# Kernel tuning notes

Hardware: AMD Instinct MI355X
Metric: run time of the kernel (lower is better)

Reference implementation:

```python
import jax, jax.numpy as jnp
import numpy as np

B = 4096
N_WIRES = 4
N_OPS = 8
# fixed (control, target) wire pairs for the 8 'random' two-qubit CRY gates
PAIRS = [(0, 1), (1, 2), (2, 3), (3, 0), (0, 2), (1, 3), (2, 0), (3, 1)]
AX = "abcd"  # einsum letters for the 4 qubit axes


def _cry(theta):
    """Controlled-RY gate as a [2,2,2,2] tensor (c_out, t_out, c_in, t_in). Real-valued."""
    c, s = jnp.cos(theta / 2), jnp.sin(theta / 2)
    ry = jnp.stack([jnp.stack([c, -s]), jnp.stack([s, c])])  # [2,2]
    G = jnp.zeros((2, 2, 2, 2), dtype=ry.dtype)
    G = G.at[0, :, 0, :].set(jnp.eye(2, dtype=ry.dtype))
    G = G.at[1, :, 1, :].set(ry)
    return G


def _apply_2q(state, G, c, t):
    """Apply 2-qubit gate G to qubits (c, t) of state [N,2,2,2,2]."""
    out = list(AX)
    out[c], out[t] = "x", "y"
    spec = f"xy{AX[c]}{AX[t]},n{AX}->n{''.join(out)}"
    return jnp.einsum(spec, G, state)


def _quanv(x, theta):
    """Batched 4-qubit state-vector sim over all 196 2x2 patches at once."""
    bsz = x.shape[0]
    img = x.reshape(bsz, 28, 28)
    # [B,14,14,2,2] patches; flatten row-major gives [x[r,c], x[r,c+1], x[r+1,c], x[r+1,c+1]]
    patches = img.reshape(bsz, 14, 2, 14, 2).transpose(0, 1, 3, 2, 4)
    angles = patches.reshape(bsz * 196, 4)  # [N,4] RY angles
    # RY(theta)|0> = cos(t/2)|0> + sin(t/2)|1>  -> product state over 4 wires
    amp = jnp.stack([jnp.cos(angles / 2), jnp.sin(angles / 2)], axis=-1)  # [N,4,2]
    state = jnp.einsum("na,nb,nc,nd->nabcd", amp[:, 0], amp[:, 1], amp[:, 2], amp[:, 3])
    # 8 fixed-pattern parameterized CRY gates (RandomLayer analogue; all-real so state stays real)
    for k, (cw, tw) in enumerate(PAIRS):
        state = _apply_2q(state, _cry(theta[k]), cw, tw)
    probs = state ** 2  # real amplitudes -> |amp|^2
    z = jnp.array([1.0, -1.0], dtype=state.dtype)
    meas = jnp.stack([jnp.einsum(f"n{AX},{AX[w]}->n", probs, z) for w in range(N_WIRES)], axis=-1)
    return meas.reshape(bsz, 196 * 4)  # [B,784], patch-major layout matches torch cat


def setup_inputs() -> dict:
    key = jax.random.key(0)
    ks = jax.random.split(key, 11)
    x = jax.random.uniform(ks[0], (B, 1, 28, 28), dtype=jnp.float32)
    theta = jax.random.uniform(ks[1], (N_OPS,), dtype=jnp.float32, minval=0.0, maxval=2.0 * np.pi)
    s = 0.05
    W1 = jax.random.normal(ks[2], (784, 512), jnp.float32) * s
    b1 = jnp.zeros((512,), jnp.float32)
    W2 = jax.random.normal(ks[3], (512, 32), jnp.float32) * s
    b2 = jnp.zeros((32,), jnp.float32)
    W3 = jax.random.normal(ks[4], (32, 512), jnp.float32) * s
    b3 = jnp.zeros((512,), jnp.float32)
    W4 = jax.random.normal(ks[5], (512, 784), jnp.float32) * s
    b4 = jnp.zeros((784,), jnp.float32)
    return dict(x=x, theta=theta, W1=W1, b1=b1, W2=W2, b2=b2, W3=W3, b3=b3, W4=W4, b4=b4)


def reference(x, theta, W1, b1, W2, b2, W3, b3, W4, b4):
    feats = _quanv(x, theta)                          # [B,784]
    h = jax.nn.relu(feats @ W1 + b1)                  # encoder
    latent = h @ W2 + b2                              # [B,32]
    h2 = jax.nn.relu(latent @ W3 + b3)                # decoder
    recon = jax.nn.sigmoid(h2 @ W4 + b4)              # [B,784]
    return recon.reshape(x.shape[0], 1, 28, 28)
```

## Files before the change

kernel.cpp:

```cpp
#include <hip/hip_runtime.h>
#include <hip/hip_bf16.h>
#include <math.h>


#define BATCH   4096
#define NPATCH  196
#define FEATDIM 784
#define KP1     896
#define NP4     832

typedef __bf16 b8 __attribute__((ext_vector_type(8)));
typedef float  f4 __attribute__((ext_vector_type(4)));

__device__ __forceinline__ unsigned short f2bf(float f) {
    unsigned u = __float_as_uint(f);
    u += 0x7FFF + ((u >> 16) & 1);
    return (unsigned short)(u >> 16);
}

__device__ __forceinline__ void gload16(const void* g, void* l) {
    __builtin_amdgcn_global_load_lds(
        (const __attribute__((address_space(1))) unsigned int*)g,
        (__attribute__((address_space(3))) unsigned int*)l, 16, 0, 0);
}

#define Q_END   3136
#define T1_END  3248
#define T4_END  3352
#define W2T_END 3416
#define W3T_END 3480
#define ZF_END  3704

__global__ __launch_bounds__(256)
void prep_kernel(const float* __restrict__ x, const float* __restrict__ theta,
                 const float* __restrict__ W1, const float* __restrict__ W2,
                 const float* __restrict__ W3, const float* __restrict__ W4,
                 unsigned short* __restrict__ featsB,
                 unsigned short* __restrict__ W1B,
                 unsigned short* __restrict__ W4B,
                 unsigned short* __restrict__ W2T,
                 unsigned short* __restrict__ W3T) {
    __shared__ float shm[64 * 65];
    const int bid = blockIdx.x;
    const int tid = threadIdx.x;

    if (bid < Q_END) {
        float (*Us)[16] = (float (*)[16])shm;
        if (tid < 16) {
            const int cb[8] = {3, 2, 1, 0, 3, 2, 1, 0};
            const int tb[8] = {2, 1, 0, 3, 1, 0, 3, 2};
            float v[16];
#pragma unroll
            for (int s = 0; s < 16; ++s) v[s] = (s == tid) ? 1.0f : 0.0f;
            for (int k = 0; k < 8; ++k) {
                float th = theta[k] * 0.5f;
                float ct, st;
                __sincosf(th, &st, &ct);
                int cm = 1 << cb[k], tm = 1 << tb[k];
#pragma unroll
                for (int s = 0; s < 16; ++s) {
                    if ((s & cm) && !(s & tm)) {
                        float v0 = v[s], v1 = v[s | tm];
                        v[s]      = ct * v0 - st * v1;
                        v[s | tm] = st * v0 + ct * v1;
                    }
                }
            }
#pragma unroll
            for (int s = 0; s < 16; ++s) Us[s][tid] = v[s];
        }
        __syncthreads();

        int n = bid * 256 + tid;
        int b = n / NPATCH;
        int p = n % NPATCH;
        int r = p / 14;
        int c = p % 14;

        const float* img = x + (size_t)b * FEATDIM;
        float2 p0 = *(const float2*)&img[(2 * r) * 28 + 2 * c];
        float2 p1 = *(const float2*)&img[(2 * r + 1) * 28 + 2 * c];

        float amp[4][2];
        __sincosf(p0.x * 0.5f, &amp[0][1], &amp[0][0]);
        __sincosf(p0.y * 0.5f, &amp[1][1], &amp[1][0]);
        __sincosf(p1.x * 0.5f, &amp[2][1], &amp[2][0]);
        __sincosf(p1.y * 0.5f, &amp[3][1], &amp[3][0]);

        float av[16];
#pragma unroll
        for (int s = 0; s < 16; ++s)
            av[s] = amp[0][(s >> 3) & 1] * amp[1][(s >> 2) & 1] *
                    amp[2][(s >> 1) & 1] * amp[3][s & 1];

        float m0 = 0.f, m1 = 0.f, m2 = 0.f, m3 = 0.f;
#pragma unroll
        for (int s = 0; s < 16; ++s) {
            float vv = 0.f;
#pragma unroll
            for (int t = 0; t < 16; ++t) vv += Us[s][t] * av[t];
            float pr = vv * vv;
            m0 += ((s >> 3) & 1) ? -pr : pr;
            m1 += ((s >> 2) & 1) ? -pr : pr;
            m2 += ((s >> 1) & 1) ? -pr : pr;
            m3 += (s & 1)        ? -pr : pr;
        }
        ushort4 o;
        o.x = f2bf(m0); o.y = f2bf(m1); o.z = f2bf(m2); o.w = f2bf(m3);
        *(ushort4*)&featsB[(size_t)b * KP1 + p * 4] = o;
    } else if (bid < T1_END) {
        float (*T)[65] = (float (*)[65])shm;
        int bb = bid - Q_END;
        int k0 = (bb / 8) * 64, n0 = (bb % 8) * 64;
        int rr = tid >> 6, c = tid & 63;
#pragma unroll
        for (int i = 0; i < 16; ++i) {
            int r = i * 4 + rr;
            if (k0 + r < FEATDIM) T[r][c] = W1[(size_t)(k0 + r) * 512 + n0 + c];
        }
        __syncthreads();
#pragma unroll
        for (int i = 0; i < 16; ++i) {
            int nn = i * 4 + rr;
            unsigned short v = (k0 + c < FEATDIM) ? f2bf(T[c][nn]) : (unsigned short)0;
            W1B[(size_t)(n0 + nn) * KP1 + k0 + c] = v;
        }
    } else if (bid < T4_END) {
        float (*T)[65] = (float (*)[65])shm;
        int bb = bid - T1_END;
        int k0 = (bb / 13) * 64, n0 = (bb % 13) * 64;
        int rr = tid >> 6, c = tid & 63;
#pragma unroll
        for (int i = 0; i < 16; ++i) {
            int r = i * 4 + rr;
            T[r][c] = (n0 + c < FEATDIM) ? W4[(size_t)(k0 + r) * FEATDIM + n0 + c] : 0.f;
        }
        __syncthreads();
#pragma unroll
        for (int i = 0; i < 16; ++i) {
            int nn = i * 4 + rr;
            W4B[(size_t)(n0 + nn) * 512 + k0 + c] = f2bf(T[c][nn]);
        }
    } else if (bid < W2T_END) {
        int idx = (bid - T4_END) * 256 + tid;
        int n = idx >> 9, k = idx & 511;
        W2T[idx] = f2bf(W2[(size_t)k * 32 + n]);
    } else if (bid < W3T_END) {
        int idx = (bid - W2T_END) * 256 + tid;
        int n = idx >> 5, k = idx & 31;
        W3T[idx] = f2bf(W3[(size_t)k * 512 + n]);
    } else {
        int idx = (bid - W3T_END) * 256 + tid;
        int row = idx / 14, j = idx % 14;
        *(float4*)&featsB[(size_t)row * KP1 + FEATDIM + j * 8] =
            make_float4(0.f, 0.f, 0.f, 0.f);
    }
}

template <int ACT, int OUT_BF16>
__global__ __launch_bounds__(256)
void gemm_mfma(const unsigned short* __restrict__ A,
               const unsigned short* __restrict__ BT,
               const float* __restrict__ bias,
               void* __restrict__ C,
               int lda, int ldb, int ldc, int Nlog, int nkt, int gx) {
    __shared__ __align__(16) unsigned short As[2][2][64 * 64];
    __shared__ __align__(16) unsigned short Bs[2][2][64 * 64];

    const int nwg = gridDim.x;
    const int d   = blockIdx.x;
    const int tile = (d & 7) * (nwg >> 3) + (d >> 3);
    const int bx = tile % gx;
    const int by = tile / gx;

    const int t  = threadIdx.x;
    const int w  = t >> 6;
    const int l  = t & 63;
    const int wm = w >> 1;
    const int wn = w & 1;
    const int row0 = by * 64;
    const int col0 = bx * 64;

    const int sr = l >> 3;
    const int sc = ((l & 7) ^ sr) * 8;
    const unsigned short* Ab = A  + (size_t)(row0 + w * 8 + sr) * lda + sc;
    const unsigned short* Bb = BT + (size_t)(col0 + w * 8 + sr) * ldb + sc;

    const int q  = l >> 4;
    const int lx = l & 15;
    const int sx = l & 7;
    const int coff[2] = { ((0 + q) ^ sx) * 16, ((4 + q) ^ sx) * 16 };

    f4 acc[2][2];
#pragma unroll
    for (int m = 0; m < 2; ++m)
#pragma unroll
        for (int n = 0; n < 2; ++n) acc[m][n] = (f4)0.f;

    auto stage = [&](int bi, int kt) {
#pragma unroll
        for (int h = 0; h < 2; ++h) {
            const size_t k0 = (size_t)kt * 128 + h * 64;
            char* la = (char*)&As[bi][h][0] + w * 1024;
            char* lb = (char*)&Bs[bi][h][0] + w * 1024;
            gload16(Ab + k0, la);
            gload16(Bb + k0, lb);
            gload16(Ab + (size_t)32 * lda + k0, la + 4096);
            gload16(Bb + (size_t)32 * ldb + k0, lb + 4096);
        }
    };

    auto compute = [&](int bi) {
#pragma unroll
        for (int h = 0; h < 2; ++h) {
            const char* la = (const char*)&As[bi][h][0];
            const char* lb = (const char*)&Bs[bi][h][0];
#pragma unroll
            for (int kk = 0; kk < 2; ++kk) {
                const int co = coff[kk];
                b8 a[2], bf[2];
#pragma unroll
                for (int m = 0; m < 2; ++m)
                    a[m] = *(const b8*)(la + (wm * 32 + m * 16 + lx) * 128 + co);
#pragma unroll
                for (int n = 0; n < 2; ++n)
                    bf[n] = *(const b8*)(lb + (wn * 32 + n * 16 + lx) * 128 + co);
#pragma unroll
                for (int m = 0; m < 2; ++m)
#pragma unroll
                    for (int n = 0; n < 2; ++n)
                        acc[m][n] = __builtin_amdgcn_mfma_f32_16x16x32_bf16(
                            a[m], bf[n], acc[m][n], 0, 0, 0);
            }
        }
    };

    stage(0, 0);
    __syncthreads();
    for (int kt = 0; kt < nkt; ++kt) {
        if (kt + 1 < nkt) stage((kt + 1) & 1, kt + 1);
        compute(kt & 1);
        __syncthreads();
    }

#pragma unroll
    for (int n = 0; n < 2; ++n) {
        int col = col0 + wn * 32 + n * 16 + lx;
        if (col >= Nlog) continue;
        float bv = bias[col];
#pragma unroll
        for (int m = 0; m < 2; ++m) {
            int row = row0 + wm * 32 + m * 16 + q * 4;
#pragma unroll
            for (int r = 0; r < 4; ++r) {
                float v = acc[m][n][r] + bv;
                if (ACT == 1) v = fmaxf(v, 0.f);
                if (ACT == 2) v = 1.0f / (1.0f + __expf(-v));
                if (OUT_BF16)
                    ((unsigned short*)C)[(size_t)(row + r) * ldc + col] = f2bf(v);
                else
                    __builtin_nontemporal_store(
                        v, &((float*)C)[(size_t)(row + r) * ldc + col]);
            }
        }
    }
}

__global__ __launch_bounds__(256)
void mlp_mid(const unsigned short* __restrict__ h1B,
             const unsigned short* __restrict__ W2T,
             const unsigned short* __restrict__ W3T,
             const float* __restrict__ b2,
             const float* __restrict__ b3,
             unsigned short* __restrict__ h2B) {
    __shared__ float part[64][34];

    const int t  = threadIdx.x;
    const int w  = t >> 6;
    const int l  = t & 63;
    const int q  = l >> 4;
    const int lx = l & 15;
    const int row0 = blockIdx.x * 16;

    f4 acc0 = (f4)0.f, acc1 = (f4)0.f;
#pragma unroll
    for (int s = 0; s < 4; ++s) {
        const int k0 = w * 128 + s * 32 + q * 8;
        b8 a   = *(const b8*)&h1B[(size_t)(row0 + lx) * 512 + k0];
        b8 bf0 = *(const b8*)&W2T[(size_t)lx * 512 + k0];
        b8 bf1 = *(const b8*)&W2T[(size_t)(16 + lx) * 512 + k0];
        acc0 = __builtin_amdgcn_mfma_f32_16x16x32_bf16(a, bf0, acc0, 0, 0, 0);
        acc1 = __builtin_amdgcn_mfma_f32_16x16x32_bf16(a, bf1, acc1, 0, 0, 0);
    }
#pragma unroll
    for (int r = 0; r < 4; ++r) {
        part[w * 16 + q * 4 + r][lx]      = acc0[r];
        part[w * 16 + q * 4 + r][16 + lx] = acc1[r];
    }
    __syncthreads();

    union { unsigned short us[8]; b8 v; } au;
#pragma unroll
    for (int j = 0; j < 8; ++j) {
        const int c = q * 8 + j;
        float s = b2[c];
#pragma unroll
        for (int ww = 0; ww < 4; ++ww) s += part[ww * 16 + lx][c];
        au.us[j] = f2bf(s);
    }
    const b8 a2 = au.v;

#pragma unroll
    for (int jg = 0; jg < 8; ++jg) {
        const int col = (w * 8 + jg) * 16 + lx;
        b8 bf = *(const b8*)&W3T[(size_t)col * 32 + q * 8];
        f4 o = __builtin_amdgcn_mfma_f32_16x16x32_bf16(a2, bf, (f4)0.f, 0, 0, 0);
        const float bb = b3[col];
#pragma unroll
        for (int r = 0; r < 4; ++r) {
            float v = fmaxf(o[r] + bb, 0.f);
            h2B[(size_t)(row0 + q * 4 + r) * 512 + col] = f2bf(v);
        }
    }
}

extern "C" void kernel_launch(void* const* d_in, const int* in_sizes, int n_in,
                              void* d_out, int out_size, void* d_ws, size_t ws_size,
                              hipStream_t stream) {
    const float* x     = (const float*)d_in[0];
    const float* theta = (const float*)d_in[1];
    const float* W1    = (const float*)d_in[2];
    const float* b1    = (const float*)d_in[3];
    const float* W2    = (const float*)d_in[4];
    const float* b2    = (const float*)d_in[5];
    const float* W3    = (const float*)d_in[6];
    const float* b3    = (const float*)d_in[7];
    const float* W4    = (const float*)d_in[8];
    const float* b4    = (const float*)d_in[9];
    float* out = (float*)d_out;

    char* ws = (char*)d_ws;
    unsigned short* featsB = (unsigned short*)ws;   ws += (size_t)BATCH * KP1 * 2;
    unsigned short* W1B    = (unsigned short*)ws;   ws += (size_t)512 * KP1 * 2;
    unsigned short* W4B    = (unsigned short*)ws;   ws += (size_t)NP4 * 512 * 2;
    unsigned short* W2T    = (unsigned short*)ws;   ws += (size_t)32 * 512 * 2;
    unsigned short* W3T    = (unsigned short*)ws;   ws += (size_t)512 * 32 * 2;
    unsigned short* h1B    = (unsigned short*)ws;   ws += (size_t)BATCH * 512 * 2;
    unsigned short* h2B    = (unsigned short*)ws;

    prep_kernel<<<ZF_END, 256, 0, stream>>>(
        x, theta, W1, W2, W3, W4, featsB, W1B, W4B, W2T, W3T);

    gemm_mfma<1, 1><<<512, 256, 0, stream>>>(
        featsB, W1B, b1, h1B, KP1, KP1, 512, 512, KP1 / 128, 8);
    mlp_mid<<<256, 256, 0, stream>>>(h1B, W2T, W3T, b2, b3, h2B);
    gemm_mfma<2, 0><<<832, 256, 0, stream>>>(
        h2B, W4B, b4, out, 512, 512, FEATDIM, FEATDIM, 4, 13);
}
```

Baseline: 53.26 us.

## Shrink GEMM1 K padding to 832 and move W4 transpose into mlp_mid

The padded K dimension of the first GEMM drops from 896 to 832, and the last K tile now loads and computes only its first 64-wide half, so less zero padding is read and multiplied. The W4 transpose/bf16 conversion moves out of the prep kernel into extra blocks of the small mlp_mid launch, where that launch has spare capacity. The staging and compute loops lose their unroll pragma and gain a runtime half-tile branch, which may cost some scheduling quality. Padding-zero blocks are also reduced.

```diff
diff --git a/kernel.cpp b/kernel.cpp
--- a/kernel.cpp
+++ b/kernel.cpp
@@ -6,7 +6,7 @@
 #define BATCH   4096
 #define NPATCH  196
 #define FEATDIM 784
-#define KP1     896
+#define KP1     832
 #define NP4     832
 
 typedef __bf16 b8 __attribute__((ext_vector_type(8)));
@@ -25,19 +25,17 @@
 }
 
 #define Q_END   3136
-#define T1_END  3248
-#define T4_END  3352
-#define W2T_END 3416
-#define W3T_END 3480
-#define ZF_END  3704
+#define T1_END  3240
+#define W2T_END 3304
+#define W3T_END 3368
+#define ZF_END  3464
 
 __global__ __launch_bounds__(256)
 void prep_kernel(const float* __restrict__ x, const float* __restrict__ theta,
                  const float* __restrict__ W1, const float* __restrict__ W2,
-                 const float* __restrict__ W3, const float* __restrict__ W4,
+                 const float* __restrict__ W3,
                  unsigned short* __restrict__ featsB,
                  unsigned short* __restrict__ W1B,
-                 unsigned short* __restrict__ W4B,
                  unsigned short* __restrict__ W2T,
                  unsigned short* __restrict__ W3T) {
     __shared__ float shm[64 * 65];
@@ -125,24 +123,8 @@
             unsigned short v = (k0 + c < FEATDIM) ? f2bf(T[c][nn]) : (unsigned short)0;
             W1B[(size_t)(n0 + nn) * KP1 + k0 + c] = v;
         }
-    } else if (bid < T4_END) {
-        float (*T)[65] = (float (*)[65])shm;
-        int bb = bid - T1_END;
-        int k0 = (bb / 13) * 64, n0 = (bb % 13) * 64;
-        int rr = tid >> 6, c = tid & 63;
-#pragma unroll
-        for (int i = 0; i < 16; ++i) {
-            int r = i * 4 + rr;
-            T[r][c] = (n0 + c < FEATDIM) ? W4[(size_t)(k0 + r) * FEATDIM + n0 + c] : 0.f;
-        }
-        __syncthreads();
-#pragma unroll
-        for (int i = 0; i < 16; ++i) {
-            int nn = i * 4 + rr;
-            W4B[(size_t)(n0 + nn) * 512 + k0 + c] = f2bf(T[c][nn]);
-        }
     } else if (bid < W2T_END) {
-        int idx = (bid - T4_END) * 256 + tid;
+        int idx = (bid - T1_END) * 256 + tid;
         int n = idx >> 9, k = idx & 511;
         W2T[idx] = f2bf(W2[(size_t)k * 32 + n]);
     } else if (bid < W3T_END) {
@@ -151,7 +133,7 @@
         W3T[idx] = f2bf(W3[(size_t)k * 512 + n]);
     } else {
         int idx = (bid - W3T_END) * 256 + tid;
-        int row = idx / 14, j = idx % 14;
+        int row = idx / 6, j = idx % 6;
         *(float4*)&featsB[(size_t)row * KP1 + FEATDIM + j * 8] =
             make_float4(0.f, 0.f, 0.f, 0.f);
     }
@@ -163,7 +145,8 @@
                const unsigned short* __restrict__ BT,
                const float* __restrict__ bias,
                void* __restrict__ C,
-               int lda, int ldb, int ldc, int Nlog, int nkt, int gx) {
+               int lda, int ldb, int ldc, int Nlog, int nkt, int khalf,
+               int gx) {
     __shared__ __align__(16) unsigned short As[2][2][64 * 64];
     __shared__ __align__(16) unsigned short Bs[2][2][64 * 64];
 
@@ -198,8 +181,8 @@
         for (int n = 0; n < 2; ++n) acc[m][n] = (f4)0.f;
 
     auto stage = [&](int bi, int kt) {
-#pragma unroll
-        for (int h = 0; h < 2; ++h) {
+        const int nh = (khalf && kt == nkt - 1) ? 1 : 2;
+        for (int h = 0; h < nh; ++h) {
             const size_t k0 = (size_t)kt * 128 + h * 64;
             char* la = (char*)&As[bi][h][0] + w * 1024;
             char* lb = (char*)&Bs[bi][h][0] + w * 1024;
@@ -210,9 +193,9 @@
         }
     };
 
-    auto compute = [&](int bi) {
-#pragma unroll
-        for (int h = 0; h < 2; ++h) {
+    auto compute = [&](int bi, int kt) {
+        const int nh = (khalf && kt == nkt - 1) ? 1 : 2;
+        for (int h = 0; h < nh; ++h) {
             const char* la = (const char*)&As[bi][h][0];
             const char* lb = (const char*)&Bs[bi][h][0];
 #pragma unroll
@@ -239,7 +222,7 @@
     __syncthreads();
     for (int kt = 0; kt < nkt; ++kt) {
         if (kt + 1 < nkt) stage((kt + 1) & 1, kt + 1);
-        compute(kt & 1);
+        compute(kt & 1, kt);
         __syncthreads();
     }
 
@@ -272,10 +255,33 @@
              const unsigned short* __restrict__ W3T,
              const float* __restrict__ b2,
              const float* __restrict__ b3,
-             unsigned short* __restrict__ h2B) {
-    __shared__ float part[64][34];
+             const float* __restrict__ W4,
+             unsigned short* __restrict__ h2B,
+             unsigned short* __restrict__ W4B) {
+    __shared__ float shm[64 * 65];
 
     const int t  = threadIdx.x;
+
+    if (blockIdx.x >= 256) {
+        float (*T)[65] = (float (*)[65])shm;
+        int bb = blockIdx.x - 256;
+        int k0 = (bb / 13) * 64, n0 = (bb % 13) * 64;
+        int rr = t >> 6, c = t & 63;
+#pragma unroll
+        for (int i = 0; i < 16; ++i) {
+            int r = i * 4 + rr;
+            T[r][c] = (n0 + c < FEATDIM) ? W4[(size_t)(k0 + r) * FEATDIM + n0 + c] : 0.f;
+        }
+        __syncthreads();
+#pragma unroll
+        for (int i = 0; i < 16; ++i) {
+            int nn = i * 4 + rr;
+            W4B[(size_t)(n0 + nn) * 512 + k0 + c] = f2bf(T[c][nn]);
+        }
+        return;
+    }
+
+    float (*part)[34] = (float (*)[34])shm;
     const int w  = t >> 6;
     const int l  = t & 63;
     const int q  = l >> 4;
@@ -349,11 +355,11 @@
     unsigned short* h2B    = (unsigned short*)ws;
 
     prep_kernel<<<ZF_END, 256, 0, stream>>>(
-        x, theta, W1, W2, W3, W4, featsB, W1B, W4B, W2T, W3T);
+        x, theta, W1, W2, W3, featsB, W1B, W2T, W3T);
 
     gemm_mfma<1, 1><<<512, 256, 0, stream>>>(
-        featsB, W1B, b1, h1B, KP1, KP1, 512, 512, KP1 / 128, 8);
-    mlp_mid<<<256, 256, 0, stream>>>(h1B, W2T, W3T, b2, b3, h2B);
+        featsB, W1B, b1, h1B, KP1, KP1, 512, 512, 7, 1, 8);
+    mlp_mid<<<360, 256, 0, stream>>>(h1B, W2T, W3T, b2, b3, W4, h2B, W4B);
     gemm_mfma<2, 0><<<832, 256, 0, stream>>>(
-        h2B, W4B, b4, out, 512, 512, FEATDIM, FEATDIM, 4, 13);
-}
+        h2B, W4B, b4, out, 512, 512, FEATDIM, FEATDIM, 4, 0, 13);
+}
```

Result: no change. 53.34 us (+0.2%).
